# Kernel optimization log

Hardware: AMD Instinct MI355X
Metric: run time of the kernel (lower is better)

The kernel has to match this reference:

```python
import jax, jax.numpy as jnp
import numpy as np

ALPHA = 0.2  # leaky relu slope
NEG_BIG = -9000000000000000.0


def setup_inputs() -> dict:
    key = jax.random.key(0)
    k1, k2, k3, k4 = jax.random.split(key, 4)
    B, N, Fin, Fout = 8, 2048, 256, 256
    h = jax.random.normal(k1, (B, N, Fin), dtype=jnp.float32)
    adj = jax.random.randint(k2, (B, N, N), 0, 2, dtype=jnp.int32)
    # xavier_uniform with gain=1.414
    gain = 1.414
    limW = gain * np.sqrt(6.0 / (Fin + Fout))
    W = jax.random.uniform(k3, (Fin, Fout), dtype=jnp.float32, minval=-limW, maxval=limW)
    lima = gain * np.sqrt(6.0 / (2 * Fout + 1))
    a = jax.random.uniform(k4, (2 * Fout, 1), dtype=jnp.float32, minval=-lima, maxval=lima)
    return {"h": h, "adj": adj, "W": W, "a": a}


def reference(h, adj, W, a):
    # Wh: [B, N, F]
    Wh = jnp.matmul(h, W)
    Fout = W.shape[1]
    a1 = a[:Fout, 0]   # scores for source node i (repeat_interleave side)
    a2 = a[Fout:, 0]   # scores for target node j (repeat side)
    # e[b,i,j] = leakyrelu(Wh[b,i]@a1 + Wh[b,j]@a2)  -- decomposed, no O(N^2 * 2F) tensor
    s1 = jnp.einsum('bnf,f->bn', Wh, a1)  # [B, N]
    s2 = jnp.einsum('bnf,f->bn', Wh, a2)  # [B, N]
    e = jax.nn.leaky_relu(s1[:, :, None] + s2[:, None, :], negative_slope=ALPHA)
    masked = jnp.where(adj > 0, e, jnp.full_like(e, NEG_BIG))
    attention = jax.nn.softmax(masked, axis=2)  # dropout=0 (eval mode)
    h_prime = jnp.matmul(attention, Wh)  # [B, N, F]
    return jax.nn.elu(h_prime)
```

## Files before the change

kernel.cpp:

```cpp
#include <hip/hip_runtime.h>

typedef __attribute__((ext_vector_type(8))) short bhalf8;
typedef __attribute__((ext_vector_type(4))) float floatx4;

#define ALPHA_LR 0.2f

__device__ __forceinline__ unsigned short f2bf(float f) {
  union { float f; unsigned int u; } v; v.f = f;
  unsigned int r = v.u + 0x7fffu + ((v.u >> 16) & 1u);
  return (unsigned short)(r >> 16);
}
__device__ __forceinline__ float bf2f(unsigned short u) {
  union { unsigned int u; float f; } v; v.u = ((unsigned int)u) << 16;
  return v.f;
}
__device__ __forceinline__ void gld16(const void* g, void* l) {
  __builtin_amdgcn_global_load_lds((const __attribute__((address_space(1))) unsigned int*)g,
                                   (__attribute__((address_space(3))) unsigned int*)l,
                                   16, 0, 0);
}

__global__ void k0w_split(const float* __restrict__ W,
                          unsigned short* __restrict__ WThi,
                          unsigned short* __restrict__ WTlo,
                          unsigned int* __restrict__ s2maxEnc) {
  __shared__ float s[16][17];
  const int tx = threadIdx.x, ty = threadIdx.y;
  if (blockIdx.x == 0 && blockIdx.y == 0 && ty == 0 && tx < 8) s2maxEnc[tx] = 0u;
  const int n0 = blockIdx.x * 16, k0 = blockIdx.y * 16;
  s[ty][tx] = W[(k0 + ty) * 256 + n0 + tx];
  __syncthreads();
  float v = s[tx][ty];
  const int k = k0 + tx, n = n0 + ty;
  unsigned short hi = f2bf(v);
  unsigned short lo = f2bf(v - bf2f(hi));
  const int idx = (k >> 5) * 8192 + n * 32 + (k & 31);
  WThi[idx] = hi;
  WTlo[idx] = lo;
}

__global__ __launch_bounds__(512, 2) void k1_mfma(const float* __restrict__ h,
                                                  const unsigned short* __restrict__ Bhi_g,
                                                  const unsigned short* __restrict__ Blo_g,
                                                  const float* __restrict__ a_g,
                                                  unsigned short* __restrict__ WhPack,
                                                  float* __restrict__ s1,
                                                  float* __restrict__ s2,
                                                  unsigned int* __restrict__ s2maxEnc) {
  __shared__ unsigned short Ah[64 * 264];
  __shared__ unsigned short Bh[2][8192], Bl[2][8192];
  __shared__ float s1red[64], s2red[64];
  const int t = threadIdx.x;
  const long r0 = (long)blockIdx.x * 64;
  const int wave = t >> 6, lane = t & 63;

  if (t < 64) { s1red[t] = 0.f; s2red[t] = 0.f; }

#pragma unroll
  for (int rep = 0; rep < 2; rep++) {
    const int off = wave * 1024 + rep * 512;
    gld16(Bhi_g + off + lane * 8, &Bh[0][off]);
    gld16(Blo_g + off + lane * 8, &Bl[0][off]);
  }

#pragma unroll
  for (int q = 0; q < 8; q++) {
    int idx = q * 512 + t;
    int row = idx >> 6, c4 = idx & 63;
    float4 x = *(const float4*)(h + (r0 + row) * 256 + c4 * 4);
    unsigned short hs[4] = {f2bf(x.x), f2bf(x.y), f2bf(x.z), f2bf(x.w)};
    *(ushort4*)&Ah[row * 264 + c4 * 4] = (ushort4){hs[0], hs[1], hs[2], hs[3]};
  }
  __syncthreads();

  const int wm = wave >> 2, wn = wave & 3;
  const int lhi = lane >> 4, llo = lane & 15;

  floatx4 acc[2][4];
#pragma unroll
  for (int mt = 0; mt < 2; mt++)
#pragma unroll
    for (int nt = 0; nt < 4; nt++) acc[mt][nt] = (floatx4){0.f, 0.f, 0.f, 0.f};

  for (int ks = 0; ks < 8; ks++) {
    const int cur = ks & 1, nxt = cur ^ 1, ksn = (ks + 1) & 7;
#pragma unroll
    for (int rep = 0; rep < 2; rep++) {
      const int off = wave * 1024 + rep * 512;
      gld16(Bhi_g + ksn * 8192 + off + lane * 8, &Bh[nxt][off]);
      gld16(Blo_g + ksn * 8192 + off + lane * 8, &Bl[nxt][off]);
    }

    const int k0 = ks * 32;
    bhalf8 ah[2], bh[4], bl[4];
#pragma unroll
    for (int mt = 0; mt < 2; mt++) {
      int ro = (wm * 32 + mt * 16 + llo) * 264 + k0 + lhi * 8;
      ah[mt] = *(const bhalf8*)&Ah[ro];
    }
#pragma unroll
    for (int nt = 0; nt < 4; nt++) {
      int ro = (wn * 64 + nt * 16 + llo) * 32 + lhi * 8;
      bh[nt] = *(const bhalf8*)&Bh[cur][ro];
      bl[nt] = *(const bhalf8*)&Bl[cur][ro];
    }
#pragma unroll
    for (int mt = 0; mt < 2; mt++)
#pragma unroll
      for (int nt = 0; nt < 4; nt++) {
        acc[mt][nt] = __builtin_amdgcn_mfma_f32_16x16x32_bf16(ah[mt], bh[nt], acc[mt][nt], 0, 0, 0);
        acc[mt][nt] = __builtin_amdgcn_mfma_f32_16x16x32_bf16(ah[mt], bl[nt], acc[mt][nt], 0, 0, 0);
      }
    __syncthreads();
  }

  float a1v[4], a2v[4];
#pragma unroll
  for (int nt = 0; nt < 4; nt++) {
    int f = wn * 64 + nt * 16 + llo;
    a1v[nt] = a_g[f];
    a2v[nt] = a_g[256 + f];
  }

  const int b = (int)(r0 >> 11);
  const int jt_base = (int)((r0 & 2047) >> 5);

#pragma unroll
  for (int mt = 0; mt < 2; mt++) {
    float p1[4], p2[4];
#pragma unroll
    for (int reg = 0; reg < 4; reg++) {
      p1[reg] = acc[mt][0][reg] * a1v[0] + acc[mt][1][reg] * a1v[1] +
                acc[mt][2][reg] * a1v[2] + acc[mt][3][reg] * a1v[3];
      p2[reg] = acc[mt][0][reg] * a2v[0] + acc[mt][1][reg] * a2v[1] +
                acc[mt][2][reg] * a2v[2] + acc[mt][3][reg] * a2v[3];
    }
#pragma unroll
    for (int off = 1; off < 16; off <<= 1) {
#pragma unroll
      for (int reg = 0; reg < 4; reg++) {
        p1[reg] += __shfl_xor(p1[reg], off);
        p2[reg] += __shfl_xor(p2[reg], off);
      }
    }
    if (llo == 0) {
#pragma unroll
      for (int reg = 0; reg < 4; reg++) {
        int il = wm * 32 + mt * 16 + lhi * 4 + reg;
        atomicAdd(&s1red[il], p1[reg]);
        atomicAdd(&s2red[il], p2[reg]);
      }
    }
#pragma unroll
    for (int nt = 0; nt < 4; nt++) {
      int f = wn * 64 + nt * 16 + llo;
      int jt = jt_base + wm;
      ushort4 pk = (ushort4){f2bf(acc[mt][nt][0]), f2bf(acc[mt][nt][1]),
                             f2bf(acc[mt][nt][2]), f2bf(acc[mt][nt][3])};
      *(ushort4*)&WhPack[((long)((b * 64 + jt) * 256 + f)) * 32 + mt * 16 + lhi * 4] = pk;
    }
  }

  __syncthreads();
  if (t < 64) {
    s1[r0 + t] = s1red[t];
    s2[r0 + t] = s2red[t];
    float v = s2red[t];
#pragma unroll
    for (int o = 32; o; o >>= 1) v = fmaxf(v, __shfl_xor(v, o));
    if (t == 0) {
      unsigned int u = __float_as_uint(v);
      unsigned int key = (u & 0x80000000u) ? ~u : (u | 0x80000000u);
      atomicMax(s2maxEnc + b, key);
    }
  }
}

__global__ __launch_bounds__(512, 2) void k3_attn(const unsigned short* __restrict__ WhPack,
                                                  const int* __restrict__ adj,
                                                  const float* __restrict__ s1g,
                                                  const float* __restrict__ s2g,
                                                  const unsigned int* __restrict__ s2maxEnc,
                                                  float* __restrict__ out) {
  const int t = threadIdx.x;
  const int lin = blockIdx.x;
  const int b = lin & 7;
  const int ig = lin >> 3;
  const long gr0 = (long)b * 2048 + ig * 64;

  const int wave = t >> 6, lane = t & 63;
  const int rg = wave >> 2, fg = wave & 3;
  const int llo = lane & 15, lhi = lane >> 4;

  __shared__ unsigned short WhL[2][16384];
  __shared__ unsigned short Pl[2][64 * 72];
  __shared__ float s2l[2048];
  __shared__ float lvv[64];

  const int pr = t >> 3;
  const int pq = t & 7;

  const float s1i = s1g[gr0 + pr];
  const unsigned int ek = s2maxEnc[b];
  const float s2max = (ek & 0x80000000u) ? __uint_as_float(ek & 0x7fffffffu)
                                         : __uint_as_float(~ek);
  const float xm = s1i + s2max;
  const float Mi = fmaxf(xm, ALPHA_LR * xm);
  const int* arow = adj + (gr0 + pr) * 2048 + pq * 8;

  const int gsrc8 = (((lane & 3) ^ ((lane >> 3) & 3))) * 8;
  const unsigned short* wsrcB =
      WhPack + (long)b * 524288 + wave * 512 + (lane >> 2) * 32 + gsrc8;

  const int boff = fg * 2048 + llo * 32 + (lhi ^ ((llo >> 1) & 3)) * 8;
  const int aoff = (rg * 32 + llo) * 72 + lhi * 8;

  *(float4*)&s2l[t * 4] = *(const float4*)(s2g + (long)b * 2048 + t * 4);
#pragma unroll
  for (int i = 0; i < 4; i++)
    gld16(wsrcB + i * 4096, &WhL[0][i * 4096 + wave * 512]);
  int4 a0A = *(const int4*)(arow);
  int4 a0B = *(const int4*)(arow + 4);
  int4 ajCA = *(const int4*)(arow + 64);
  int4 ajCB = *(const int4*)(arow + 68);
  __syncthreads();

  float lsum = 0.f;
  {
    int am[8] = {a0A.x, a0A.y, a0A.z, a0A.w, a0B.x, a0B.y, a0B.z, a0B.w};
    float4 sA = *(const float4*)&s2l[pq * 8];
    float4 sB = *(const float4*)&s2l[pq * 8 + 4];
    float xs[8] = {sA.x, sA.y, sA.z, sA.w, sB.x, sB.y, sB.z, sB.w};
    unsigned int pk[4];
    float e[8];
#pragma unroll
    for (int q = 0; q < 8; q++) {
      float x = s1i + xs[q];
      float lk = fmaxf(x, ALPHA_LR * x);
      float ee = __expf(lk - Mi);
      ee = (am[q] > 0) ? ee : 0.f;
      lsum += ee;
      e[q] = ee;
    }
#pragma unroll
    for (int q = 0; q < 4; q++)
      asm("v_cvt_pk_bf16_f32 %0, %1, %2" : "=v"(pk[q]) : "v"(e[2 * q]), "v"(e[2 * q + 1]));
    *(uint4*)&Pl[0][pr * 72 + pq * 8] = (uint4){pk[0], pk[1], pk[2], pk[3]};
  }
  __syncthreads();

  floatx4 acc[2][4];
#pragma unroll
  for (int mt = 0; mt < 2; mt++)
#pragma unroll
    for (int nt = 0; nt < 4; nt++) acc[mt][nt] = (floatx4){0.f, 0.f, 0.f, 0.f};

#pragma unroll 2
  for (int step = 0; step < 32; step++) {
    const int cur = step & 1, nxt = cur ^ 1;

    if (step < 31) {
      const long jb = (long)(step + 1) * 16384;
#pragma unroll
      for (int i = 0; i < 4; i++)
        gld16(wsrcB + jb + i * 4096, &WhL[nxt][i * 4096 + wave * 512]);
    }
    const int tp = (step < 30 ? step + 2 : 31) * 64;
    int4 ajNA = *(const int4*)(arow + tp);
    int4 ajNB = *(const int4*)(arow + tp + 4);
    __builtin_amdgcn_sched_barrier(0);

    if (step < 31) {
      int am[8] = {ajCA.x, ajCA.y, ajCA.z, ajCA.w, ajCB.x, ajCB.y, ajCB.z, ajCB.w};
      const int sbase = (step + 1) * 64 + pq * 8;
      float4 sA = *(const float4*)&s2l[sbase];
      float4 sB = *(const float4*)&s2l[sbase + 4];
      float xs[8] = {sA.x, sA.y, sA.z, sA.w, sB.x, sB.y, sB.z, sB.w};
      unsigned int pk[4];
      float e[8];
#pragma unroll
      for (int q = 0; q < 8; q++) {
        float x = s1i + xs[q];
        float lk = fmaxf(x, ALPHA_LR * x);
        float ee = __expf(lk - Mi);
        ee = (am[q] > 0) ? ee : 0.f;
        lsum += ee;
        e[q] = ee;
      }
#pragma unroll
      for (int q = 0; q < 4; q++)
        asm("v_cvt_pk_bf16_f32 %0, %1, %2" : "=v"(pk[q]) : "v"(e[2 * q]), "v"(e[2 * q + 1]));
      *(uint4*)&Pl[nxt][pr * 72 + pq * 8] = (uint4){pk[0], pk[1], pk[2], pk[3]};
    }
    ajCA = ajNA; ajCB = ajNB;

#pragma unroll
    for (int kk = 0; kk < 2; kk++) {
      bhalf8 aF[2], bF[4];
#pragma unroll
      for (int mt = 0; mt < 2; mt++)
        aF[mt] = *(const bhalf8*)&Pl[cur][aoff + mt * 1152 + kk * 32];
#pragma unroll
      for (int nt = 0; nt < 4; nt++)
        bF[nt] = *(const bhalf8*)&WhL[cur][kk * 8192 + nt * 512 + boff];
#pragma unroll
      for (int mt = 0; mt < 2; mt++)
#pragma unroll
        for (int nt = 0; nt < 4; nt++)
          acc[mt][nt] = __builtin_amdgcn_mfma_f32_16x16x32_bf16(aF[mt], bF[nt], acc[mt][nt], 0, 0, 0);
    }

    __syncthreads();
  }

  lsum += __shfl_xor(lsum, 1);
  lsum += __shfl_xor(lsum, 2);
  lsum += __shfl_xor(lsum, 4);
  if ((lane & 7) == 0) lvv[pr] = lsum;
  __syncthreads();

#pragma unroll
  for (int mt = 0; mt < 2; mt++) {
#pragma unroll
    for (int reg = 0; reg < 4; reg++) {
      const int rloc = rg * 32 + mt * 16 + lhi * 4 + reg;
      const float iv = 1.f / fmaxf(lvv[rloc], 1e-35f);
      const long orow = (gr0 + rloc) * 256 + fg * 64 + llo;
#pragma unroll
      for (int nt = 0; nt < 4; nt++) {
        float v = acc[mt][nt][reg] * iv;
        v = v > 0.f ? v : expm1f(v);
        out[orow + nt * 16] = v;
      }
    }
  }
}

extern "C" void kernel_launch(void* const* d_in, const int* in_sizes, int n_in,
                              void* d_out, int out_size, void* d_ws, size_t ws_size,
                              hipStream_t stream) {
  const float* h = (const float*)d_in[0];
  const int* adj = (const int*)d_in[1];
  const float* W = (const float*)d_in[2];
  const float* a = (const float*)d_in[3];
  float* out = (float*)d_out;

  char* ws = (char*)d_ws;
  unsigned short* WhPack = (unsigned short*)ws;
  unsigned short* WThi = (unsigned short*)(ws + 8388608);
  unsigned short* WTlo = (unsigned short*)(ws + 8519680);
  float* s1 = (float*)(ws + 8650752);
  float* s2 = (float*)(ws + 8716288);
  unsigned int* s2maxEnc = (unsigned int*)(ws + 8781824);

  hipLaunchKernelGGL(k0w_split, dim3(16, 16), dim3(16, 16), 0, stream, W, WThi, WTlo, s2maxEnc);
  hipLaunchKernelGGL(k1_mfma, dim3(256), dim3(512), 0, stream, h, WThi, WTlo, a,
                     WhPack, s1, s2, s2maxEnc);
  hipLaunchKernelGGL(k3_attn, dim3(256), dim3(512), 0, stream, WhPack, adj,
                     s1, s2, s2maxEnc, out);
}
```

Measured before the change: 242.4 us.

## Halve attention K-step to 32 and pipeline Wh loads with partial vmcnt waits

Restructures the attention main loop from 32 steps of 64 columns to 64 steps of 32 columns. Each wave now loads its own private 64-feature slice of Wh, and the XOR-swizzled layout is dropped. Full __syncthreads are replaced by hand-written waitcnt/barrier sequences with a partial vmcnt wait, so Wh prefetches can overlap the MFMAs. Smaller P tiles and per-step work aim to cut barrier stalls, at the cost of twice as many barriers. The unswizzled layout may also bring LDS bank conflicts and extra redundant loads on the tail step.

```diff
diff --git a/kernel.cpp b/kernel.cpp
--- a/kernel.cpp
+++ b/kernel.cpp
@@ -193,7 +193,7 @@
   const int llo = lane & 15, lhi = lane >> 4;
 
   __shared__ unsigned short WhL[2][16384];
-  __shared__ unsigned short Pl[2][64 * 72];
+  __shared__ unsigned short Pl[2][64 * 40];
   __shared__ float s2l[2048];
   __shared__ float lvv[64];
 
@@ -206,35 +206,28 @@
                                          : __uint_as_float(~ek);
   const float xm = s1i + s2max;
   const float Mi = fmaxf(xm, ALPHA_LR * xm);
-  const int* arow = adj + (gr0 + pr) * 2048 + pq * 8;
-
-  const int gsrc8 = (((lane & 3) ^ ((lane >> 3) & 3))) * 8;
-  const unsigned short* wsrcB =
-      WhPack + (long)b * 524288 + wave * 512 + (lane >> 2) * 32 + gsrc8;
-
-  const int boff = fg * 2048 + llo * 32 + (lhi ^ ((llo >> 1) & 3)) * 8;
-  const int aoff = (rg * 32 + llo) * 72 + lhi * 8;
+  const int* arow = adj + (gr0 + pr) * 2048 + pq * 4;
+
+  const unsigned short* wsrc = WhPack + (long)b * 524288 + (fg * 64) * 32 +
+                               (lane >> 2) * 32 + (lane & 3) * 8;
+  unsigned short* wdst = &WhL[0][wave * 2048];
 
   *(float4*)&s2l[t * 4] = *(const float4*)(s2g + (long)b * 2048 + t * 4);
 #pragma unroll
-  for (int i = 0; i < 4; i++)
-    gld16(wsrcB + i * 4096, &WhL[0][i * 4096 + wave * 512]);
-  int4 a0A = *(const int4*)(arow);
-  int4 a0B = *(const int4*)(arow + 4);
-  int4 ajCA = *(const int4*)(arow + 64);
-  int4 ajCB = *(const int4*)(arow + 68);
+  for (int i = 0; i < 4; i++) gld16(wsrc + i * 512, wdst + i * 512);
+  int4 aj0 = *(const int4*)(arow);
+  int4 ajC = *(const int4*)(arow + 32);
   __syncthreads();
 
   float lsum = 0.f;
   {
-    int am[8] = {a0A.x, a0A.y, a0A.z, a0A.w, a0B.x, a0B.y, a0B.z, a0B.w};
-    float4 sA = *(const float4*)&s2l[pq * 8];
-    float4 sB = *(const float4*)&s2l[pq * 8 + 4];
-    float xs[8] = {sA.x, sA.y, sA.z, sA.w, sB.x, sB.y, sB.z, sB.w};
-    unsigned int pk[4];
-    float e[8];
-#pragma unroll
-    for (int q = 0; q < 8; q++) {
+    float4 s2v = *(const float4*)&s2l[pq * 4];
+    float xs[4] = {s2v.x, s2v.y, s2v.z, s2v.w};
+    int am[4] = {aj0.x, aj0.y, aj0.z, aj0.w};
+    unsigned int pk[2];
+    float e[4];
+#pragma unroll
+    for (int q = 0; q < 4; q++) {
       float x = s1i + xs[q];
       float lk = fmaxf(x, ALPHA_LR * x);
       float ee = __expf(lk - Mi);
@@ -242,12 +235,11 @@
       lsum += ee;
       e[q] = ee;
     }
-#pragma unroll
-    for (int q = 0; q < 4; q++)
-      asm("v_cvt_pk_bf16_f32 %0, %1, %2" : "=v"(pk[q]) : "v"(e[2 * q]), "v"(e[2 * q + 1]));
-    *(uint4*)&Pl[0][pr * 72 + pq * 8] = (uint4){pk[0], pk[1], pk[2], pk[3]};
-  }
-  __syncthreads();
+    asm("v_cvt_pk_bf16_f32 %0, %1, %2" : "=v"(pk[0]) : "v"(e[0]), "v"(e[1]));
+    asm("v_cvt_pk_bf16_f32 %0, %1, %2" : "=v"(pk[1]) : "v"(e[2]), "v"(e[3]));
+    *(uint2*)&Pl[0][pr * 40 + pq * 4] = (uint2){pk[0], pk[1]};
+  }
+  asm volatile("s_waitcnt lgkmcnt(0)\n\ts_barrier" ::: "memory");
 
   floatx4 acc[2][4];
 #pragma unroll
@@ -255,62 +247,59 @@
 #pragma unroll
     for (int nt = 0; nt < 4; nt++) acc[mt][nt] = (floatx4){0.f, 0.f, 0.f, 0.f};
 
-#pragma unroll 2
-  for (int step = 0; step < 32; step++) {
+  for (int step = 0; step < 64; step++) {
     const int cur = step & 1, nxt = cur ^ 1;
-
-    if (step < 31) {
-      const long jb = (long)(step + 1) * 16384;
-#pragma unroll
-      for (int i = 0; i < 4; i++)
-        gld16(wsrcB + jb + i * 4096, &WhL[nxt][i * 4096 + wave * 512]);
-    }
-    const int tp = (step < 30 ? step + 2 : 31) * 64;
-    int4 ajNA = *(const int4*)(arow + tp);
-    int4 ajNB = *(const int4*)(arow + tp + 4);
+    const int tn = (step < 63) ? step + 1 : 63;
+    const int tp = (step < 62) ? step + 2 : 63;
+
+#pragma unroll
+    for (int i = 0; i < 4; i++)
+      gld16(wsrc + (long)tn * 8192 + i * 512,
+            &WhL[0][nxt * 16384 + wave * 2048 + i * 512]);
+    int4 ajN = *(const int4*)(arow + tp * 32);
     __builtin_amdgcn_sched_barrier(0);
 
-    if (step < 31) {
-      int am[8] = {ajCA.x, ajCA.y, ajCA.z, ajCA.w, ajCB.x, ajCB.y, ajCB.z, ajCB.w};
-      const int sbase = (step + 1) * 64 + pq * 8;
-      float4 sA = *(const float4*)&s2l[sbase];
-      float4 sB = *(const float4*)&s2l[sbase + 4];
-      float xs[8] = {sA.x, sA.y, sA.z, sA.w, sB.x, sB.y, sB.z, sB.w};
-      unsigned int pk[4];
-      float e[8];
-#pragma unroll
-      for (int q = 0; q < 8; q++) {
+    {
+      float4 s2v = *(const float4*)&s2l[tn * 32 + pq * 4];
+      float xs[4] = {s2v.x, s2v.y, s2v.z, s2v.w};
+      int am[4] = {ajC.x, ajC.y, ajC.z, ajC.w};
+      unsigned int pk[2];
+      float e[4];
+      float lsm = 0.f;
+#pragma unroll
+      for (int q = 0; q < 4; q++) {
         float x = s1i + xs[q];
         float lk = fmaxf(x, ALPHA_LR * x);
         float ee = __expf(lk - Mi);
         ee = (am[q] > 0) ? ee : 0.f;
-        lsum += ee;
+        lsm += ee;
         e[q] = ee;
       }
-#pragma unroll
-      for (int q = 0; q < 4; q++)
-        asm("v_cvt_pk_bf16_f32 %0, %1, %2" : "=v"(pk[q]) : "v"(e[2 * q]), "v"(e[2 * q + 1]));
-      *(uint4*)&Pl[nxt][pr * 72 + pq * 8] = (uint4){pk[0], pk[1], pk[2], pk[3]};
-    }
-    ajCA = ajNA; ajCB = ajNB;
-
-#pragma unroll
-    for (int kk = 0; kk < 2; kk++) {
-      bhalf8 aF[2], bF[4];
-#pragma unroll
-      for (int mt = 0; mt < 2; mt++)
-        aF[mt] = *(const bhalf8*)&Pl[cur][aoff + mt * 1152 + kk * 32];
+      if (step < 63) lsum += lsm;
+      asm("v_cvt_pk_bf16_f32 %0, %1, %2" : "=v"(pk[0]) : "v"(e[0]), "v"(e[1]));
+      asm("v_cvt_pk_bf16_f32 %0, %1, %2" : "=v"(pk[1]) : "v"(e[2]), "v"(e[3]));
+      *(uint2*)&Pl[nxt][pr * 40 + pq * 4] = (uint2){pk[0], pk[1]};
+    }
+    ajC = ajN;
+
+    asm volatile("s_waitcnt vmcnt(6)" ::: "memory");
+    __builtin_amdgcn_sched_barrier(0);
+
+    bhalf8 aF[2], bF[4];
+#pragma unroll
+    for (int mt = 0; mt < 2; mt++)
+      aF[mt] = *(const bhalf8*)&Pl[cur][(rg * 32 + mt * 16 + llo) * 40 + lhi * 8];
+#pragma unroll
+    for (int nt = 0; nt < 4; nt++)
+      bF[nt] = *(const bhalf8*)&WhL[0][cur * 16384 + wave * 2048 +
+                                       (nt * 16 + llo) * 32 + lhi * 8];
+#pragma unroll
+    for (int mt = 0; mt < 2; mt++)
 #pragma unroll
       for (int nt = 0; nt < 4; nt++)
-        bF[nt] = *(const bhalf8*)&WhL[cur][kk * 8192 + nt * 512 + boff];
-#pragma unroll
-      for (int mt = 0; mt < 2; mt++)
-#pragma unroll
-        for (int nt = 0; nt < 4; nt++)
-          acc[mt][nt] = __builtin_amdgcn_mfma_f32_16x16x32_bf16(aF[mt], bF[nt], acc[mt][nt], 0, 0, 0);
-    }
-
-    __syncthreads();
+        acc[mt][nt] = __builtin_amdgcn_mfma_f32_16x16x32_bf16(aF[mt], bF[nt], acc[mt][nt], 0, 0, 0);
+
+    asm volatile("s_waitcnt lgkmcnt(0)\n\ts_barrier" ::: "memory");
   }
 
   lsum += __shfl_xor(lsum, 1);
```

Result: slower. 264.8 us (+9.2%).

## Halve attention row tile and K step to double grid and occupancy

Applied to the files above, without the earlier changes.

Retiles the attention kernel to 32 query rows per block and 32 neighbour columns per pipeline step instead of 64, and doubles the grid to 512 blocks with a launch bound of 4 blocks per CU. The aim is more resident waves per CU to hide latency on the adjacency stream and the exp/softmax math. The cost is that each block does fewer MFMAs per barrier. The full Wh matrix is also re-read from L2 twice as often, and adjacency is loaded with narrower int2 reads.

```diff
diff --git a/kernel.cpp b/kernel.cpp
--- a/kernel.cpp
+++ b/kernel.cpp
@@ -176,7 +176,7 @@
   }
 }
 
-__global__ __launch_bounds__(512, 2) void k3_attn(const unsigned short* __restrict__ WhPack,
+__global__ __launch_bounds__(512, 4) void k3_attn(const unsigned short* __restrict__ WhPack,
                                                   const int* __restrict__ adj,
                                                   const float* __restrict__ s1g,
                                                   const float* __restrict__ s2g,
@@ -186,19 +186,19 @@
   const int lin = blockIdx.x;
   const int b = lin & 7;
   const int ig = lin >> 3;
-  const long gr0 = (long)b * 2048 + ig * 64;
+  const long gr0 = (long)b * 2048 + ig * 32;
 
   const int wave = t >> 6, lane = t & 63;
   const int rg = wave >> 2, fg = wave & 3;
   const int llo = lane & 15, lhi = lane >> 4;
 
-  __shared__ unsigned short WhL[2][16384];
-  __shared__ unsigned short Pl[2][64 * 72];
+  __shared__ unsigned short WhL[2][8192];
+  __shared__ unsigned short Pl[2][32 * 40];
   __shared__ float s2l[2048];
-  __shared__ float lvv[64];
-
-  const int pr = t >> 3;
-  const int pq = t & 7;
+  __shared__ float lvv[32];
+
+  const int pr = t >> 4;
+  const int pq = t & 15;
 
   const float s1i = s1g[gr0 + pr];
   const unsigned int ek = s2maxEnc[b];
@@ -206,35 +206,31 @@
                                          : __uint_as_float(~ek);
   const float xm = s1i + s2max;
   const float Mi = fmaxf(xm, ALPHA_LR * xm);
-  const int* arow = adj + (gr0 + pr) * 2048 + pq * 8;
+  const int* arow = adj + (gr0 + pr) * 2048 + pq * 2;
 
   const int gsrc8 = (((lane & 3) ^ ((lane >> 3) & 3))) * 8;
   const unsigned short* wsrcB =
       WhPack + (long)b * 524288 + wave * 512 + (lane >> 2) * 32 + gsrc8;
 
   const int boff = fg * 2048 + llo * 32 + (lhi ^ ((llo >> 1) & 3)) * 8;
-  const int aoff = (rg * 32 + llo) * 72 + lhi * 8;
+  const int aoff = llo * 40 + lhi * 8;
 
   *(float4*)&s2l[t * 4] = *(const float4*)(s2g + (long)b * 2048 + t * 4);
 #pragma unroll
-  for (int i = 0; i < 4; i++)
+  for (int i = 0; i < 2; i++)
     gld16(wsrcB + i * 4096, &WhL[0][i * 4096 + wave * 512]);
-  int4 a0A = *(const int4*)(arow);
-  int4 a0B = *(const int4*)(arow + 4);
-  int4 ajCA = *(const int4*)(arow + 64);
-  int4 ajCB = *(const int4*)(arow + 68);
+  int2 aj0 = *(const int2*)(arow);
+  int2 ajC = *(const int2*)(arow + 32);
   __syncthreads();
 
   float lsum = 0.f;
   {
-    int am[8] = {a0A.x, a0A.y, a0A.z, a0A.w, a0B.x, a0B.y, a0B.z, a0B.w};
-    float4 sA = *(const float4*)&s2l[pq * 8];
-    float4 sB = *(const float4*)&s2l[pq * 8 + 4];
-    float xs[8] = {sA.x, sA.y, sA.z, sA.w, sB.x, sB.y, sB.z, sB.w};
-    unsigned int pk[4];
-    float e[8];
-#pragma unroll
-    for (int q = 0; q < 8; q++) {
+    float2 s2v = *(const float2*)&s2l[pq * 2];
+    float xs[2] = {s2v.x, s2v.y};
+    int am[2] = {aj0.x, aj0.y};
+    float e[2];
+#pragma unroll
+    for (int q = 0; q < 2; q++) {
       float x = s1i + xs[q];
       float lk = fmaxf(x, ALPHA_LR * x);
       float ee = __expf(lk - Mi);
@@ -242,44 +238,37 @@
       lsum += ee;
       e[q] = ee;
     }
-#pragma unroll
-    for (int q = 0; q < 4; q++)
-      asm("v_cvt_pk_bf16_f32 %0, %1, %2" : "=v"(pk[q]) : "v"(e[2 * q]), "v"(e[2 * q + 1]));
-    *(uint4*)&Pl[0][pr * 72 + pq * 8] = (uint4){pk[0], pk[1], pk[2], pk[3]};
-  }
-  __syncthreads();
-
-  floatx4 acc[2][4];
-#pragma unroll
-  for (int mt = 0; mt < 2; mt++)
-#pragma unroll
-    for (int nt = 0; nt < 4; nt++) acc[mt][nt] = (floatx4){0.f, 0.f, 0.f, 0.f};
+    unsigned int pk;
+    asm("v_cvt_pk_bf16_f32 %0, %1, %2" : "=v"(pk) : "v"(e[0]), "v"(e[1]));
+    *(unsigned int*)&Pl[0][pr * 40 + pq * 2] = pk;
+  }
+  __syncthreads();
+
+  floatx4 acc[4];
+#pragma unroll
+  for (int nt = 0; nt < 4; nt++) acc[nt] = (floatx4){0.f, 0.f, 0.f, 0.f};
 
 #pragma unroll 2
-  for (int step = 0; step < 32; step++) {
+  for (int step = 0; step < 64; step++) {
     const int cur = step & 1, nxt = cur ^ 1;
 
-    if (step < 31) {
-      const long jb = (long)(step + 1) * 16384;
-#pragma unroll
-      for (int i = 0; i < 4; i++)
+    if (step < 63) {
+      const long jb = (long)(step + 1) * 8192;
+#pragma unroll
+      for (int i = 0; i < 2; i++)
         gld16(wsrcB + jb + i * 4096, &WhL[nxt][i * 4096 + wave * 512]);
     }
-    const int tp = (step < 30 ? step + 2 : 31) * 64;
-    int4 ajNA = *(const int4*)(arow + tp);
-    int4 ajNB = *(const int4*)(arow + tp + 4);
+    const int tp = (step < 62 ? step + 2 : 63);
+    int2 ajN = *(const int2*)(arow + tp * 32);
     __builtin_amdgcn_sched_barrier(0);
 
-    if (step < 31) {
-      int am[8] = {ajCA.x, ajCA.y, ajCA.z, ajCA.w, ajCB.x, ajCB.y, ajCB.z, ajCB.w};
-      const int sbase = (step + 1) * 64 + pq * 8;
-      float4 sA = *(const float4*)&s2l[sbase];
-      float4 sB = *(const float4*)&s2l[sbase + 4];
-      float xs[8] = {sA.x, sA.y, sA.z, sA.w, sB.x, sB.y, sB.z, sB.w};
-      unsigned int pk[4];
-      float e[8];
-#pragma unroll
-      for (int q = 0; q < 8; q++) {
+    if (step < 63) {
+      float2 s2v = *(const float2*)&s2l[(step + 1) * 32 + pq * 2];
+      float xs[2] = {s2v.x, s2v.y};
+      int am[2] = {ajC.x, ajC.y};
+      float e[2];
+#pragma unroll
+      for (int q = 0; q < 2; q++) {
         float x = s1i + xs[q];
         float lk = fmaxf(x, ALPHA_LR * x);
         float ee = __expf(lk - Mi);
@@ -287,28 +276,20 @@
         lsum += ee;
         e[q] = ee;
       }
-#pragma unroll
-      for (int q = 0; q < 4; q++)
-        asm("v_cvt_pk_bf16_f32 %0, %1, %2" : "=v"(pk[q]) : "v"(e[2 * q]), "v"(e[2 * q + 1]));
-      *(uint4*)&Pl[nxt][pr * 72 + pq * 8] = (uint4){pk[0], pk[1], pk[2], pk[3]};
-    }
-    ajCA = ajNA; ajCB = ajNB;
-
-#pragma unroll
-    for (int kk = 0; kk < 2; kk++) {
-      bhalf8 aF[2], bF[4];
-#pragma unroll
-      for (int mt = 0; mt < 2; mt++)
-        aF[mt] = *(const bhalf8*)&Pl[cur][aoff + mt * 1152 + kk * 32];
-#pragma unroll
-      for (int nt = 0; nt < 4; nt++)
-        bF[nt] = *(const bhalf8*)&WhL[cur][kk * 8192 + nt * 512 + boff];
-#pragma unroll
-      for (int mt = 0; mt < 2; mt++)
-#pragma unroll
-        for (int nt = 0; nt < 4; nt++)
-          acc[mt][nt] = __builtin_amdgcn_mfma_f32_16x16x32_bf16(aF[mt], bF[nt], acc[mt][nt], 0, 0, 0);
-    }
+      unsigned int pk;
+      asm("v_cvt_pk_bf16_f32 %0, %1, %2" : "=v"(pk) : "v"(e[0]), "v"(e[1]));
+      *(unsigned int*)&Pl[nxt][pr * 40 + pq * 2] = pk;
+    }
+    ajC = ajN;
+
+    bhalf8 aF = *(const bhalf8*)&Pl[cur][rg * 16 * 40 + aoff];
+    bhalf8 bF[4];
+#pragma unroll
+    for (int nt = 0; nt < 4; nt++)
+      bF[nt] = *(const bhalf8*)&WhL[cur][nt * 512 + boff];
+#pragma unroll
+    for (int nt = 0; nt < 4; nt++)
+      acc[nt] = __builtin_amdgcn_mfma_f32_16x16x32_bf16(aF, bF[nt], acc[nt], 0, 0, 0);
 
     __syncthreads();
   }
@@ -316,22 +297,20 @@
   lsum += __shfl_xor(lsum, 1);
   lsum += __shfl_xor(lsum, 2);
   lsum += __shfl_xor(lsum, 4);
-  if ((lane & 7) == 0) lvv[pr] = lsum;
-  __syncthreads();
-
-#pragma unroll
-  for (int mt = 0; mt < 2; mt++) {
-#pragma unroll
-    for (int reg = 0; reg < 4; reg++) {
-      const int rloc = rg * 32 + mt * 16 + lhi * 4 + reg;
-      const float iv = 1.f / fmaxf(lvv[rloc], 1e-35f);
-      const long orow = (gr0 + rloc) * 256 + fg * 64 + llo;
-#pragma unroll
-      for (int nt = 0; nt < 4; nt++) {
-        float v = acc[mt][nt][reg] * iv;
-        v = v > 0.f ? v : expm1f(v);
-        out[orow + nt * 16] = v;
-      }
+  lsum += __shfl_xor(lsum, 8);
+  if ((lane & 15) == 0) lvv[pr] = lsum;
+  __syncthreads();
+
+#pragma unroll
+  for (int reg = 0; reg < 4; reg++) {
+    const int rloc = rg * 16 + lhi * 4 + reg;
+    const float iv = 1.f / fmaxf(lvv[rloc], 1e-35f);
+    const long orow = (gr0 + rloc) * 256 + fg * 64 + llo;
+#pragma unroll
+    for (int nt = 0; nt < 4; nt++) {
+      float v = acc[nt][reg] * iv;
+      v = v > 0.f ? v : expm1f(v);
+      out[orow + nt * 16] = v;
     }
   }
 }
@@ -356,6 +335,6 @@
   hipLaunchKernelGGL(k0w_split, dim3(16, 16), dim3(16, 16), 0, stream, W, WThi, WTlo, s2maxEnc);
   hipLaunchKernelGGL(k1_mfma, dim3(256), dim3(512), 0, stream, h, WThi, WTlo, a,
                      WhPack, s1, s2, s2maxEnc);
-  hipLaunchKernelGGL(k3_attn, dim3(256), dim3(512), 0, stream, WhPack, adj,
+  hipLaunchKernelGGL(k3_attn, dim3(512), dim3(512), 0, stream, WhPack, adj,
                      s1, s2, s2maxEnc, out);
 }
```

Result: slower. 251.1 us (+3.6%).
